# Optimization experiments

Measured on AMD Instinct MI355X. Metric: run time of the kernel, lower is better.

## Reference

```python
import jax, jax.numpy as jnp
import numpy as np

N_NODES = 100000
N_EDGES = 1600000
D_IN = 128
D_H = 128
NEG_SLOPE = 0.2  # DGL GATConv default


def gat_layer(x, W, attn_l, attn_r, bias, src, dst, n_nodes):
    # x: [N, Din] -> h: [N, H]  (num_heads=1, head dim squeezed)
    h = x @ W
    el = jnp.einsum('nh,h->n', h, attn_l)  # [N]
    er = jnp.einsum('nh,h->n', h, attn_r)  # [N]
    e = jax.nn.leaky_relu(el[src] + er[dst], NEG_SLOPE)  # [E]
    # edge softmax over incoming edges of each dst node (numerically stable)
    m = jax.ops.segment_max(e, dst, num_segments=n_nodes)  # [N], -inf on zero-in-degree
    ex = jnp.exp(e - m[dst])  # [E]
    s = jax.ops.segment_sum(ex, dst, num_segments=n_nodes)  # [N]
    a = ex / s[dst]  # [E]
    out = jax.ops.segment_sum(a[:, None] * h[src], dst, num_segments=n_nodes)  # [N, H]
    return out + bias


def setup_inputs() -> dict:
    key = jax.random.key(0)
    ks = jax.random.split(key, 16)
    feat = jax.random.normal(ks[0], (N_NODES, D_IN), dtype=jnp.float32)
    src = jax.random.randint(ks[1], (N_EDGES,), 0, N_NODES, dtype=jnp.int32)
    dst = jax.random.randint(ks[2], (N_EDGES,), 0, N_NODES, dtype=jnp.int32)
    def xavier(k, shape):
        fan = sum(shape)
        return jax.random.normal(k, shape, dtype=jnp.float32) * jnp.sqrt(2.0 / fan)
    params = {}
    dims = [D_IN, D_H, D_H]
    for i in range(3):
        params[f'W{i+1}'] = xavier(ks[3 + 4 * i], (dims[i], D_H))
        params[f'al{i+1}'] = xavier(ks[4 + 4 * i], (D_H,))
        params[f'ar{i+1}'] = xavier(ks[5 + 4 * i], (D_H,))
        params[f'b{i+1}'] = jnp.zeros((D_H,), dtype=jnp.float32)
    return dict(feat=feat, src=src, dst=dst, **params)


def reference(feat, src, dst, W1, al1, ar1, b1, W2, al2, ar2, b2, W3, al3, ar3, b3):
    n = feat.shape[0]
    h = gat_layer(feat, W1, al1, ar1, b1, src, dst, n)
    h = gat_layer(h, W2, al2, ar2, b2, src, dst, n)
    h = gat_layer(h, W3, al3, ar3, b3, src, dst, n)
    return h  # [N, H] (head dim of size 1 squeezed)
```

## Files before the change

kernel.cpp:

```cpp
#include <hip/hip_runtime.h>

#define DH 128
#define NBMAX 1024
#define BCH 16384

typedef __attribute__((ext_vector_type(8))) short s16x8;
typedef __attribute__((ext_vector_type(4))) float f32x4;
typedef __attribute__((ext_vector_type(4))) uint u32x4;

__device__ __forceinline__ ushort f2bf(float x) {
  uint u = __builtin_bit_cast(uint, x);
  u = (u + 0x7FFF + ((u >> 16) & 1)) >> 16;
  return (ushort)u;
}
__device__ __forceinline__ float bfl2f(uint u) {
  return __builtin_bit_cast(float, u << 16);
}
__device__ __forceinline__ float bfh2f(uint u) {
  return __builtin_bit_cast(float, u & 0xFFFF0000u);
}


__global__ __launch_bounds__(256) void chist_kernel(const int* __restrict__ dst,
                                                    int* __restrict__ chist, int E, int NB) {
  __shared__ int h[NBMAX];
  int t = threadIdx.x;
  for (int i = t; i < NB; i += 256) h[i] = 0;
  __syncthreads();
  int base = blockIdx.x * BCH;
  int n = min(BCH, E - base);
  for (int i = t; i < n; i += 256) atomicAdd(&h[((uint)dst[base + i]) >> 7], 1);
  __syncthreads();
  for (int i = t; i < NB; i += 256)
    if (h[i]) atomicAdd(&chist[i * 16], h[i]);
}

__global__ __launch_bounds__(256) void cscan_kernel(const int* __restrict__ chist,
                                                    int* __restrict__ cbase, int* __restrict__ ccur,
                                                    int* __restrict__ rowptr, int N, int NB, int E) {
  __shared__ int lds[256];
  int t = threadIdx.x;
  int v[4], s = 0;
#pragma unroll
  for (int j = 0; j < 4; ++j) {
    int idx = t * 4 + j;
    v[j] = (idx < NB) ? chist[idx * 16] : 0;
    s += v[j];
  }
  lds[t] = s;
  __syncthreads();
  for (int off = 1; off < 256; off <<= 1) {
    int add = (t >= off) ? lds[t - off] : 0;
    __syncthreads();
    lds[t] += add;
    __syncthreads();
  }
  int run = t ? lds[t - 1] : 0;
#pragma unroll
  for (int j = 0; j < 4; ++j) {
    int idx = t * 4 + j;
    if (idx < NB) {
      cbase[idx] = run;
      ccur[idx * 16] = run;
    }
    run += v[j];
  }
  if (t == 255) cbase[NB] = lds[255];
  if (t == 0) rowptr[N] = E;
}

__global__ __launch_bounds__(256) void binscat_kernel(const int* __restrict__ src,
                                                      const int* __restrict__ dst,
                                                      int* __restrict__ ccur,
                                                      uint* __restrict__ puv, int E, int NB) {
  __shared__ int h[NBMAX];
  __shared__ int gb[NBMAX];
  int t = threadIdx.x;
  int base = blockIdx.x * BCH;
  int n = min(BCH, E - base);
  for (int i = t; i < NB; i += 256) h[i] = 0;
  __syncthreads();
  for (int i = t; i < n; i += 256) atomicAdd(&h[((uint)dst[base + i]) >> 7], 1);
  __syncthreads();
  for (int i = t; i < NB; i += 256) {
    int c = h[i];
    gb[i] = c ? atomicAdd(&ccur[i * 16], c) : 0;
    h[i] = 0;
  }
  __syncthreads();
  for (int i = t; i < n; i += 256) {
    uint d = (uint)dst[base + i];
    int b = d >> 7;
    int p = gb[b] + atomicAdd(&h[b], 1);
    puv[p] = ((d & 127u) << 25) | (uint)src[base + i];
  }
}

__global__ __launch_bounds__(256) void finesort_kernel(const uint* __restrict__ puv,
                                                       const int* __restrict__ cbase,
                                                       int* __restrict__ rowptr,
                                                       int* __restrict__ ssrc, int N) {
  int b = blockIdx.x;
  int base = cbase[b];
  int cnt = cbase[b + 1] - base;
  __shared__ int ncnt[128], nincl[128], noff[128];
  int t = threadIdx.x;
  if (t < 128) ncnt[t] = 0;
  __syncthreads();
  for (int i = t; i < cnt; i += 256) atomicAdd(&ncnt[puv[base + i] >> 25], 1);
  __syncthreads();
  if (t < 128) nincl[t] = ncnt[t];
  __syncthreads();
  for (int off = 1; off < 128; off <<= 1) {
    int add = (t < 128 && t >= off) ? nincl[t - off] : 0;
    __syncthreads();
    if (t < 128) nincl[t] += add;
    __syncthreads();
  }
  if (t < 128) {
    noff[t] = nincl[t] - ncnt[t];
    int node = (b << 7) + t;
    if (node < N) rowptr[node] = base + noff[t];
    ncnt[t] = 0;
  }
  __syncthreads();
  for (int i = t; i < cnt; i += 256) {
    uint e = puv[base + i];
    int ln = e >> 25;
    int p = base + noff[ln] + atomicAdd(&ncnt[ln], 1);
    ssrc[p] = (int)(e & 0x1FFFFFFu);
  }
}

__global__ __launch_bounds__(256) void wt_kernel(const float* __restrict__ W0,
                                                 const float* __restrict__ W1,
                                                 const float* __restrict__ W2,
                                                 ushort* __restrict__ Wtb) {
  int b = blockIdx.x;
  int layer = b >> 6;
  const float* W = layer == 0 ? W0 : (layer == 1 ? W1 : W2);
  int i = (b & 63) * 256 + threadIdx.x;
  int col = i >> 7, k = i & 127;
  Wtb[(size_t)layer * DH * DH + (size_t)col * DH + k] = f2bf(W[(size_t)k * DH + col]);
}

template <bool XF32>
__global__ __launch_bounds__(512) void gemm_kernel(const void* __restrict__ xin,
                                                   const ushort* __restrict__ Wtb,
                                                   const float* __restrict__ al,
                                                   const float* __restrict__ ar,
                                                   ushort* __restrict__ hb,
                                                   float* __restrict__ el,
                                                   float* __restrict__ er, int M) {
  __shared__ ushort As[128 * DH];
  __shared__ ushort Bs[DH * DH];
  int t = threadIdx.x;
  int R0 = blockIdx.x * 128;

  for (int i = t; i < 2048; i += 512) {
    int col = i >> 4, kb = i & 15;
    s16x8 v = *(const s16x8*)(Wtb + (size_t)col * DH + kb * 8);
    *(s16x8*)(&Bs[col * DH + ((kb ^ (col & 15)) * 8)]) = v;
  }
  for (int i = t; i < 2048; i += 512) {
    int row = i >> 4, kb = i & 15;
    int gr = R0 + row;
    s16x8 v;
    if (gr < M) {
      if constexpr (XF32) {
        const float4* p = (const float4*)((const float*)xin + (size_t)gr * DH + kb * 8);
        float4 a = p[0], b = p[1];
        v[0] = (short)f2bf(a.x); v[1] = (short)f2bf(a.y);
        v[2] = (short)f2bf(a.z); v[3] = (short)f2bf(a.w);
        v[4] = (short)f2bf(b.x); v[5] = (short)f2bf(b.y);
        v[6] = (short)f2bf(b.z); v[7] = (short)f2bf(b.w);
      } else {
        v = *(const s16x8*)((const ushort*)xin + (size_t)gr * DH + kb * 8);
      }
    } else {
      v = (s16x8)0;
    }
    *(s16x8*)(&As[row * DH + ((kb ^ (row & 15)) * 8)]) = v;
  }
  __syncthreads();

  int w = t >> 6, lane = t & 63;
  int li = lane & 15, lq = lane >> 4;
  f32x4 acc[8] = {};
  int arow = w * 16 + li;
#pragma unroll
  for (int kc = 0; kc < 4; ++kc) {
    int kb = kc * 4 + lq;
    s16x8 af = *(const s16x8*)(&As[arow * DH + ((kb ^ (arow & 15)) * 8)]);
#pragma unroll
    for (int cf = 0; cf < 8; ++cf) {
      int bcol = cf * 16 + li;
      s16x8 bf = *(const s16x8*)(&Bs[bcol * DH + ((kb ^ (bcol & 15)) * 8)]);
      acc[cf] = __builtin_amdgcn_mfma_f32_16x16x32_bf16(af, bf, acc[cf], 0, 0, 0);
    }
  }

  int Rw = R0 + w * 16;
  float alv[8], arv[8];
#pragma unroll
  for (int cf = 0; cf < 8; ++cf) {
    alv[cf] = al[cf * 16 + li];
    arv[cf] = ar[cf * 16 + li];
  }
#pragma unroll
  for (int r = 0; r < 4; ++r) {
    float sl = 0.f, sr = 0.f;
#pragma unroll
    for (int cf = 0; cf < 8; ++cf) {
      sl += acc[cf][r] * alv[cf];
      sr += acc[cf][r] * arv[cf];
    }
#pragma unroll
    for (int off = 1; off <= 8; off <<= 1) {
      sl += __shfl_xor(sl, off);
      sr += __shfl_xor(sr, off);
    }
    int grow = Rw + lq * 4 + r;
    if (li == 0 && grow < M) {
      el[grow] = sl;
      er[grow] = sr;
    }
  }

  ushort* hl = &As[w * 16 * DH];
#pragma unroll
  for (int cf = 0; cf < 8; ++cf)
#pragma unroll
    for (int r = 0; r < 4; ++r) hl[(lq * 4 + r) * DH + cf * 16 + li] = f2bf(acc[cf][r]);
#pragma unroll
  for (int p = 0; p < 4; ++p) {
    int row = lane >> 2;
    int blk = (lane & 3) + p * 4;
    s16x8 v = *(const s16x8*)(&hl[row * DH + blk * 8]);
    int grow = Rw + row;
    if (grow < M)
      __builtin_nontemporal_store(v, (s16x8*)(hb + (size_t)grow * DH + blk * 8));
  }
}

template <int FINAL>
__global__ __launch_bounds__(256) void agg_kernel(const ushort* __restrict__ hb,
                                                  const float* __restrict__ el,
                                                  const float* __restrict__ er,
                                                  const int* __restrict__ rowptr,
                                                  const int* __restrict__ ssrc,
                                                  const float* __restrict__ bias,
                                                  void* __restrict__ outv, int M) {
  int wid = (blockIdx.x * blockDim.x + threadIdx.x) >> 6;
  int lane = threadIdx.x & 63;
  if (wid >= M) return;
  int begin = rowptr[wid], end = rowptr[wid + 1];
  int deg = end - begin;

  if (deg > 64) {
    float er_d = er[wid];
    float mx = -1e30f;
    for (int e = begin + lane; e < end; e += 64) {
      float s = el[ssrc[e]] + er_d;
      s = s > 0.f ? s : 0.2f * s;
      mx = fmaxf(mx, s);
    }
#pragma unroll
    for (int off = 32; off; off >>= 1) mx = fmaxf(mx, __shfl_xor(mx, off));
    float acc0 = 0.f, acc1 = 0.f, ssum_l = 0.f;
    for (int base = begin; base < end; base += 64) {
      int n = min(64, end - base);
      int e = base + lane;
      int idx = 0;
      float wgt = 0.f;
      if (lane < n) {
        idx = ssrc[e];
        float sc = el[idx] + er_d;
        sc = sc > 0.f ? sc : 0.2f * sc;
        wgt = __expf(sc - mx);
      }
      ssum_l += wgt;
      for (int j = 0; j < n; ++j) {
        int s = __shfl(idx, j);
        float wg = __shfl(wgt, j);
        uint u = ((const uint*)(hb + (size_t)s * DH))[lane];
        acc0 += wg * bfl2f(u);
        acc1 += wg * bfh2f(u);
      }
    }
#pragma unroll
    for (int off = 32; off; off >>= 1) ssum_l += __shfl_xor(ssum_l, off);
    float inv = 1.f / ssum_l;
    float2 b2 = ((const float2*)bias)[lane];
    float o0 = acc0 * inv + b2.x;
    float o1 = acc1 * inv + b2.y;
    if constexpr (FINAL) {
      ((float2*)((float*)outv + (size_t)wid * DH))[lane] = make_float2(o0, o1);
    } else {
      uint p = (uint)f2bf(o0) | ((uint)f2bf(o1) << 16);
      ((uint*)((ushort*)outv + (size_t)wid * DH))[lane] = p;
    }
    return;
  }

  float acc[8] = {};
  float inv = 0.f;
  if (deg > 0) {
    int e = begin + lane;
    int idx = (e < end) ? ssrc[e] : 0;
    float sc = -1e30f;
    if (e < end) {
      sc = el[idx] + er[wid];
      sc = sc > 0.f ? sc : 0.2f * sc;
    }
    float mx = sc;
#pragma unroll
    for (int off = 32; off; off >>= 1) mx = fmaxf(mx, __shfl_xor(mx, off));
    float wgt = (e < end) ? __expf(sc - mx) : 0.f;
    float ssum = wgt;
#pragma unroll
    for (int off = 32; off; off >>= 1) ssum += __shfl_xor(ssum, off);
    inv = 1.f / ssum;

    int q = lane >> 4, cl = lane & 15;
    const uint4* hb4 = (const uint4*)hb;
    for (int j = 0; j < deg; j += 16) {
      uint4 u[4];
      float wq[4];
#pragma unroll
      for (int k = 0; k < 4; ++k) {
        int ej = j + k * 4 + q;
        int s = __shfl(idx, ej);
        wq[k] = __shfl(wgt, ej);
        u[k] = hb4[(size_t)s * 16 + cl];
      }
#pragma unroll
      for (int k = 0; k < 4; ++k) {
        acc[0] += wq[k] * bfl2f(u[k].x); acc[1] += wq[k] * bfh2f(u[k].x);
        acc[2] += wq[k] * bfl2f(u[k].y); acc[3] += wq[k] * bfh2f(u[k].y);
        acc[4] += wq[k] * bfl2f(u[k].z); acc[5] += wq[k] * bfh2f(u[k].z);
        acc[6] += wq[k] * bfl2f(u[k].w); acc[7] += wq[k] * bfh2f(u[k].w);
      }
    }
#pragma unroll
    for (int i = 0; i < 8; ++i) {
      acc[i] += __shfl_xor(acc[i], 16);
      acc[i] += __shfl_xor(acc[i], 32);
    }
  }
  if (lane < 16) {
    float4 b0 = ((const float4*)bias)[lane * 2];
    float4 b1 = ((const float4*)bias)[lane * 2 + 1];
    float o[8];
    o[0] = acc[0] * inv + b0.x; o[1] = acc[1] * inv + b0.y;
    o[2] = acc[2] * inv + b0.z; o[3] = acc[3] * inv + b0.w;
    o[4] = acc[4] * inv + b1.x; o[5] = acc[5] * inv + b1.y;
    o[6] = acc[6] * inv + b1.z; o[7] = acc[7] * inv + b1.w;
    if constexpr (FINAL) {
      f32x4 p0 = {o[0], o[1], o[2], o[3]};
      f32x4 p1 = {o[4], o[5], o[6], o[7]};
      float* op = (float*)outv + (size_t)wid * DH + lane * 8;
      *(f32x4*)op = p0;
      *(f32x4*)(op + 4) = p1;
    } else {
      u32x4 p;
      p.x = (uint)f2bf(o[0]) | ((uint)f2bf(o[1]) << 16);
      p.y = (uint)f2bf(o[2]) | ((uint)f2bf(o[3]) << 16);
      p.z = (uint)f2bf(o[4]) | ((uint)f2bf(o[5]) << 16);
      p.w = (uint)f2bf(o[6]) | ((uint)f2bf(o[7]) << 16);
      __builtin_nontemporal_store(p, (u32x4*)((ushort*)outv + (size_t)wid * DH) + lane);
    }
  }
}

extern "C" void kernel_launch(void* const* d_in, const int* in_sizes, int n_in,
                              void* d_out, int out_size, void* d_ws, size_t ws_size,
                              hipStream_t stream) {
  const float* feat = (const float*)d_in[0];
  const int* src = (const int*)d_in[1];
  const int* dst = (const int*)d_in[2];
  const int N = in_sizes[0] / DH;
  const int E = in_sizes[1];
  const int NB = (N + 127) >> 7;
  const float* W[3]  = {(const float*)d_in[3], (const float*)d_in[7],  (const float*)d_in[11]};
  const float* al[3] = {(const float*)d_in[4], (const float*)d_in[8],  (const float*)d_in[12]};
  const float* ar[3] = {(const float*)d_in[5], (const float*)d_in[9],  (const float*)d_in[13]};
  const float* bi[3] = {(const float*)d_in[6], (const float*)d_in[10], (const float*)d_in[14]};

  char* ws = (char*)d_ws;
  size_t off = 0;
  auto alloc = [&](size_t bytes) {
    void* p = ws + off;
    off = (off + bytes + 255) & ~(size_t)255;
    return p;
  };
  ushort* hb   = (ushort*)alloc((size_t)N * DH * sizeof(ushort));
  ushort* xb   = (ushort*)alloc((size_t)N * DH * sizeof(ushort));
  float* el    = (float*)alloc((size_t)N * sizeof(float));
  float* er    = (float*)alloc((size_t)N * sizeof(float));
  int* rowptr  = (int*)alloc((size_t)(N + 1) * sizeof(int));
  int* ssrc    = (int*)alloc((size_t)E * sizeof(int));
  ushort* Wtb  = (ushort*)alloc((size_t)3 * DH * DH * sizeof(ushort));
  int* chist   = (int*)alloc((size_t)NBMAX * 16 * sizeof(int));
  int* cbase   = (int*)alloc((size_t)(NBMAX + 1) * sizeof(int));
  int* ccur    = (int*)alloc((size_t)NBMAX * 16 * sizeof(int));
  uint* puv    = (uint*)hb;

  hipMemsetAsync(chist, 0, (size_t)NBMAX * 16 * sizeof(int), stream);
  int ebl = (E + BCH - 1) / BCH;
  chist_kernel<<<ebl, 256, 0, stream>>>(dst, chist, E, NB);
  cscan_kernel<<<1, 256, 0, stream>>>(chist, cbase, ccur, rowptr, N, NB, E);
  binscat_kernel<<<ebl, 256, 0, stream>>>(src, dst, ccur, puv, E, NB);
  finesort_kernel<<<NB, 256, 0, stream>>>(puv, cbase, rowptr, ssrc, N);
  wt_kernel<<<192, 256, 0, stream>>>(W[0], W[1], W[2], Wtb);

  for (int l = 0; l < 3; ++l) {
    const ushort* Wl = Wtb + (size_t)l * DH * DH;
    if (l == 0)
      gemm_kernel<true><<<(N + 127) / 128, 512, 0, stream>>>(feat, Wl, al[l], ar[l], hb, el, er, N);
    else
      gemm_kernel<false><<<(N + 127) / 128, 512, 0, stream>>>(xb, Wl, al[l], ar[l], hb, el, er, N);
    if (l < 2)
      agg_kernel<0><<<(N + 3) / 4, 256, 0, stream>>>(hb, el, er, rowptr, ssrc, bi[l], xb, N);
    else
      agg_kernel<1><<<(N + 3) / 4, 256, 0, stream>>>(hb, el, er, rowptr, ssrc, bi[l], d_out, N);
  }
}
```

Before: 345.4 us.

## Fuse CSR histogram into layer-0 GEMM launch and merge prep kernels

Merges the weight transpose with the zeroing of the histogram into one prep kernel, replacing the memset. The destination histogram becomes extra blocks of the first-layer GEMM launch so the two overlap. The scatter scratch buffer moves from hb to xb so the GEMM output can be written before sorting. BCH shrinks to 4096 for more blocks, and the sort loops are unrolled to batch loads ahead of the LDS atomics. This adds kernel complexity and more global atomics on chist.

```diff
diff --git a/kernel.cpp b/kernel.cpp
--- a/kernel.cpp
+++ b/kernel.cpp
@@ -2,11 +2,12 @@
 
 #define DH 128
 #define NBMAX 1024
-#define BCH 16384
+#define BCH 4096
 
 typedef __attribute__((ext_vector_type(8))) short s16x8;
 typedef __attribute__((ext_vector_type(4))) float f32x4;
 typedef __attribute__((ext_vector_type(4))) uint u32x4;
+typedef __attribute__((ext_vector_type(4))) int i32x4;
 
 __device__ __forceinline__ ushort f2bf(float x) {
   uint u = __builtin_bit_cast(uint, x);
@@ -20,143 +21,32 @@
   return __builtin_bit_cast(float, u & 0xFFFF0000u);
 }
 
-
-__global__ __launch_bounds__(256) void chist_kernel(const int* __restrict__ dst,
-                                                    int* __restrict__ chist, int E, int NB) {
-  __shared__ int h[NBMAX];
-  int t = threadIdx.x;
-  for (int i = t; i < NB; i += 256) h[i] = 0;
-  __syncthreads();
-  int base = blockIdx.x * BCH;
-  int n = min(BCH, E - base);
-  for (int i = t; i < n; i += 256) atomicAdd(&h[((uint)dst[base + i]) >> 7], 1);
-  __syncthreads();
-  for (int i = t; i < NB; i += 256)
-    if (h[i]) atomicAdd(&chist[i * 16], h[i]);
-}
-
-__global__ __launch_bounds__(256) void cscan_kernel(const int* __restrict__ chist,
-                                                    int* __restrict__ cbase, int* __restrict__ ccur,
-                                                    int* __restrict__ rowptr, int N, int NB, int E) {
-  __shared__ int lds[256];
-  int t = threadIdx.x;
-  int v[4], s = 0;
-#pragma unroll
-  for (int j = 0; j < 4; ++j) {
-    int idx = t * 4 + j;
-    v[j] = (idx < NB) ? chist[idx * 16] : 0;
-    s += v[j];
-  }
-  lds[t] = s;
-  __syncthreads();
-  for (int off = 1; off < 256; off <<= 1) {
-    int add = (t >= off) ? lds[t - off] : 0;
-    __syncthreads();
-    lds[t] += add;
-    __syncthreads();
-  }
-  int run = t ? lds[t - 1] : 0;
-#pragma unroll
-  for (int j = 0; j < 4; ++j) {
-    int idx = t * 4 + j;
-    if (idx < NB) {
-      cbase[idx] = run;
-      ccur[idx * 16] = run;
-    }
-    run += v[j];
-  }
-  if (t == 255) cbase[NB] = lds[255];
-  if (t == 0) rowptr[N] = E;
-}
-
-__global__ __launch_bounds__(256) void binscat_kernel(const int* __restrict__ src,
-                                                      const int* __restrict__ dst,
-                                                      int* __restrict__ ccur,
-                                                      uint* __restrict__ puv, int E, int NB) {
-  __shared__ int h[NBMAX];
-  __shared__ int gb[NBMAX];
-  int t = threadIdx.x;
-  int base = blockIdx.x * BCH;
-  int n = min(BCH, E - base);
-  for (int i = t; i < NB; i += 256) h[i] = 0;
-  __syncthreads();
-  for (int i = t; i < n; i += 256) atomicAdd(&h[((uint)dst[base + i]) >> 7], 1);
-  __syncthreads();
-  for (int i = t; i < NB; i += 256) {
-    int c = h[i];
-    gb[i] = c ? atomicAdd(&ccur[i * 16], c) : 0;
-    h[i] = 0;
-  }
-  __syncthreads();
-  for (int i = t; i < n; i += 256) {
-    uint d = (uint)dst[base + i];
-    int b = d >> 7;
-    int p = gb[b] + atomicAdd(&h[b], 1);
-    puv[p] = ((d & 127u) << 25) | (uint)src[base + i];
-  }
-}
-
-__global__ __launch_bounds__(256) void finesort_kernel(const uint* __restrict__ puv,
-                                                       const int* __restrict__ cbase,
-                                                       int* __restrict__ rowptr,
-                                                       int* __restrict__ ssrc, int N) {
-  int b = blockIdx.x;
-  int base = cbase[b];
-  int cnt = cbase[b + 1] - base;
-  __shared__ int ncnt[128], nincl[128], noff[128];
-  int t = threadIdx.x;
-  if (t < 128) ncnt[t] = 0;
-  __syncthreads();
-  for (int i = t; i < cnt; i += 256) atomicAdd(&ncnt[puv[base + i] >> 25], 1);
-  __syncthreads();
-  if (t < 128) nincl[t] = ncnt[t];
-  __syncthreads();
-  for (int off = 1; off < 128; off <<= 1) {
-    int add = (t < 128 && t >= off) ? nincl[t - off] : 0;
-    __syncthreads();
-    if (t < 128) nincl[t] += add;
-    __syncthreads();
-  }
-  if (t < 128) {
-    noff[t] = nincl[t] - ncnt[t];
-    int node = (b << 7) + t;
-    if (node < N) rowptr[node] = base + noff[t];
-    ncnt[t] = 0;
-  }
-  __syncthreads();
-  for (int i = t; i < cnt; i += 256) {
-    uint e = puv[base + i];
-    int ln = e >> 25;
-    int p = base + noff[ln] + atomicAdd(&ncnt[ln], 1);
-    ssrc[p] = (int)(e & 0x1FFFFFFu);
-  }
-}
-
-__global__ __launch_bounds__(256) void wt_kernel(const float* __restrict__ W0,
-                                                 const float* __restrict__ W1,
-                                                 const float* __restrict__ W2,
-                                                 ushort* __restrict__ Wtb) {
-  int b = blockIdx.x;
-  int layer = b >> 6;
-  const float* W = layer == 0 ? W0 : (layer == 1 ? W1 : W2);
-  int i = (b & 63) * 256 + threadIdx.x;
-  int col = i >> 7, k = i & 127;
-  Wtb[(size_t)layer * DH * DH + (size_t)col * DH + k] = f2bf(W[(size_t)k * DH + col]);
+__global__ __launch_bounds__(512) void prep_kernel(const float* __restrict__ W0,
+                                                   const float* __restrict__ W1,
+                                                   const float* __restrict__ W2,
+                                                   ushort* __restrict__ Wtb,
+                                                   int* __restrict__ chist) {
+  int b = blockIdx.x, t = threadIdx.x;
+  if (b < 96) {
+    int g = b * 512 + t;
+    int layer = g >> 14, i = g & 16383;
+    const float* W = layer == 0 ? W0 : (layer == 1 ? W1 : W2);
+    int col = i >> 7, k = i & 127;
+    Wtb[(size_t)layer * DH * DH + (size_t)col * DH + k] = f2bf(W[(size_t)k * DH + col]);
+  } else {
+    int idx = ((b - 96) * 512 + t) * 4;
+    *(i32x4*)(chist + idx) = (i32x4){0, 0, 0, 0};
+  }
 }
 
 template <bool XF32>
-__global__ __launch_bounds__(512) void gemm_kernel(const void* __restrict__ xin,
-                                                   const ushort* __restrict__ Wtb,
-                                                   const float* __restrict__ al,
-                                                   const float* __restrict__ ar,
-                                                   ushort* __restrict__ hb,
-                                                   float* __restrict__ el,
-                                                   float* __restrict__ er, int M) {
-  __shared__ ushort As[128 * DH];
-  __shared__ ushort Bs[DH * DH];
-  int t = threadIdx.x;
-  int R0 = blockIdx.x * 128;
-
+__device__ __forceinline__ void gemm_body(ushort* __restrict__ As, ushort* __restrict__ Bs,
+                                          const void* __restrict__ xin,
+                                          const ushort* __restrict__ Wtb,
+                                          const float* __restrict__ al,
+                                          const float* __restrict__ ar,
+                                          ushort* __restrict__ hb, float* __restrict__ el,
+                                          float* __restrict__ er, int M, int R0, int t) {
   for (int i = t; i < 2048; i += 512) {
     int col = i >> 4, kb = i & 15;
     s16x8 v = *(const s16x8*)(Wtb + (size_t)col * DH + kb * 8);
@@ -240,6 +130,203 @@
     int grow = Rw + row;
     if (grow < M)
       __builtin_nontemporal_store(v, (s16x8*)(hb + (size_t)grow * DH + blk * 8));
+  }
+}
+
+__global__ __launch_bounds__(512) void gemm_kernel(const ushort* __restrict__ xin,
+                                                   const ushort* __restrict__ Wtb,
+                                                   const float* __restrict__ al,
+                                                   const float* __restrict__ ar,
+                                                   ushort* __restrict__ hb,
+                                                   float* __restrict__ el,
+                                                   float* __restrict__ er, int M) {
+  __shared__ ushort As[128 * DH];
+  __shared__ ushort Bs[DH * DH];
+  gemm_body<false>(As, Bs, xin, Wtb, al, ar, hb, el, er, M, blockIdx.x * 128, threadIdx.x);
+}
+
+__global__ __launch_bounds__(512) void gemm0_chist_kernel(const float* __restrict__ feat,
+                                                          const ushort* __restrict__ Wtb,
+                                                          const float* __restrict__ al,
+                                                          const float* __restrict__ ar,
+                                                          ushort* __restrict__ hb,
+                                                          float* __restrict__ el,
+                                                          float* __restrict__ er, int M,
+                                                          const int* __restrict__ dst,
+                                                          int* __restrict__ chist, int E, int NB,
+                                                          int GB) {
+  __shared__ ushort As[128 * DH];
+  __shared__ ushort Bs[DH * DH];
+  int b = blockIdx.x, t = threadIdx.x;
+  if (b < GB) {
+    gemm_body<true>(As, Bs, feat, Wtb, al, ar, hb, el, er, M, b * 128, t);
+    return;
+  }
+  int* h = (int*)As;
+  for (int i = t; i < NB; i += 512) h[i] = 0;
+  __syncthreads();
+  int base = (b - GB) * BCH;
+  int n = min(BCH, E - base);
+  for (int i0 = 0; i0 < n; i0 += 2048) {
+    uint d[4]; bool ok[4];
+#pragma unroll
+    for (int k = 0; k < 4; ++k) {
+      int i = i0 + k * 512 + t;
+      ok[k] = i < n;
+      d[k] = ok[k] ? (uint)dst[base + i] : 0u;
+    }
+#pragma unroll
+    for (int k = 0; k < 4; ++k)
+      if (ok[k]) atomicAdd(&h[d[k] >> 7], 1);
+  }
+  __syncthreads();
+  for (int i = t; i < NB; i += 512)
+    if (h[i]) atomicAdd(&chist[i * 16], h[i]);
+}
+
+__global__ __launch_bounds__(256) void cscan_kernel(const int* __restrict__ chist,
+                                                    int* __restrict__ cbase, int* __restrict__ ccur,
+                                                    int* __restrict__ rowptr, int N, int NB, int E) {
+  __shared__ int lds[256];
+  int t = threadIdx.x;
+  int v[4], s = 0;
+#pragma unroll
+  for (int j = 0; j < 4; ++j) {
+    int idx = t * 4 + j;
+    v[j] = (idx < NB) ? chist[idx * 16] : 0;
+    s += v[j];
+  }
+  lds[t] = s;
+  __syncthreads();
+  for (int off = 1; off < 256; off <<= 1) {
+    int add = (t >= off) ? lds[t - off] : 0;
+    __syncthreads();
+    lds[t] += add;
+    __syncthreads();
+  }
+  int run = t ? lds[t - 1] : 0;
+#pragma unroll
+  for (int j = 0; j < 4; ++j) {
+    int idx = t * 4 + j;
+    if (idx < NB) {
+      cbase[idx] = run;
+      ccur[idx * 16] = run;
+    }
+    run += v[j];
+  }
+  if (t == 255) cbase[NB] = lds[255];
+  if (t == 0) rowptr[N] = E;
+}
+
+__global__ __launch_bounds__(256) void binscat_kernel(const int* __restrict__ src,
+                                                      const int* __restrict__ dst,
+                                                      int* __restrict__ ccur,
+                                                      uint* __restrict__ puv, int E, int NB) {
+  __shared__ int h[NBMAX];
+  __shared__ int gb[NBMAX];
+  int t = threadIdx.x;
+  int base = blockIdx.x * BCH;
+  int n = min(BCH, E - base);
+  for (int i = t; i < NB; i += 256) h[i] = 0;
+  __syncthreads();
+  for (int i0 = 0; i0 < n; i0 += 2048) {
+    uint d[8]; bool ok[8];
+#pragma unroll
+    for (int k = 0; k < 8; ++k) {
+      int i = i0 + k * 256 + t;
+      ok[k] = i < n;
+      d[k] = ok[k] ? (uint)dst[base + i] : 0u;
+    }
+#pragma unroll
+    for (int k = 0; k < 8; ++k)
+      if (ok[k]) atomicAdd(&h[d[k] >> 7], 1);
+  }
+  __syncthreads();
+  for (int i = t; i < NB; i += 256) {
+    int c = h[i];
+    gb[i] = c ? atomicAdd(&ccur[i * 16], c) : 0;
+    h[i] = 0;
+  }
+  __syncthreads();
+  for (int i0 = 0; i0 < n; i0 += 2048) {
+    uint d[8], s[8]; bool ok[8];
+#pragma unroll
+    for (int k = 0; k < 8; ++k) {
+      int i = i0 + k * 256 + t;
+      ok[k] = i < n;
+      d[k] = ok[k] ? (uint)dst[base + i] : 0u;
+      s[k] = ok[k] ? (uint)src[base + i] : 0u;
+    }
+    int p[8];
+#pragma unroll
+    for (int k = 0; k < 8; ++k)
+      if (ok[k]) {
+        int bb = d[k] >> 7;
+        p[k] = gb[bb] + atomicAdd(&h[bb], 1);
+      }
+#pragma unroll
+    for (int k = 0; k < 8; ++k)
+      if (ok[k]) puv[p[k]] = ((d[k] & 127u) << 25) | s[k];
+  }
+}
+
+__global__ __launch_bounds__(256) void finesort_kernel(const uint* __restrict__ puv,
+                                                       const int* __restrict__ cbase,
+                                                       int* __restrict__ rowptr,
+                                                       int* __restrict__ ssrc, int N) {
+  int b = blockIdx.x;
+  int base = cbase[b];
+  int cnt = cbase[b + 1] - base;
+  __shared__ int ncnt[128], nincl[128], noff[128];
+  int t = threadIdx.x;
+  if (t < 128) ncnt[t] = 0;
+  __syncthreads();
+  for (int i0 = 0; i0 < cnt; i0 += 2048) {
+    uint e[8]; bool ok[8];
+#pragma unroll
+    for (int k = 0; k < 8; ++k) {
+      int i = i0 + k * 256 + t;
+      ok[k] = i < cnt;
+      e[k] = ok[k] ? puv[base + i] : 0u;
+    }
+#pragma unroll
+    for (int k = 0; k < 8; ++k)
+      if (ok[k]) atomicAdd(&ncnt[e[k] >> 25], 1);
+  }
+  __syncthreads();
+  if (t < 128) nincl[t] = ncnt[t];
+  __syncthreads();
+  for (int off = 1; off < 128; off <<= 1) {
+    int add = (t < 128 && t >= off) ? nincl[t - off] : 0;
+    __syncthreads();
+    if (t < 128) nincl[t] += add;
+    __syncthreads();
+  }
+  if (t < 128) {
+    noff[t] = nincl[t] - ncnt[t];
+    int node = (b << 7) + t;
+    if (node < N) rowptr[node] = base + noff[t];
+    ncnt[t] = 0;
+  }
+  __syncthreads();
+  for (int i0 = 0; i0 < cnt; i0 += 2048) {
+    uint e[8]; bool ok[8];
+#pragma unroll
+    for (int k = 0; k < 8; ++k) {
+      int i = i0 + k * 256 + t;
+      ok[k] = i < cnt;
+      e[k] = ok[k] ? puv[base + i] : 0u;
+    }
+    int p[8];
+#pragma unroll
+    for (int k = 0; k < 8; ++k)
+      if (ok[k]) {
+        int ln = e[k] >> 25;
+        p[k] = base + noff[ln] + atomicAdd(&ncnt[ln], 1);
+      }
+#pragma unroll
+    for (int k = 0; k < 8; ++k)
+      if (ok[k]) ssrc[p[k]] = (int)(e[k] & 0x1FFFFFFu);
   }
 }
 
@@ -404,25 +491,21 @@
   int* chist   = (int*)alloc((size_t)NBMAX * 16 * sizeof(int));
   int* cbase   = (int*)alloc((size_t)(NBMAX + 1) * sizeof(int));
   int* ccur    = (int*)alloc((size_t)NBMAX * 16 * sizeof(int));
-  uint* puv    = (uint*)hb;
-
-  hipMemsetAsync(chist, 0, (size_t)NBMAX * 16 * sizeof(int), stream);
+  uint* puv    = (uint*)xb;
+
   int ebl = (E + BCH - 1) / BCH;
-  chist_kernel<<<ebl, 256, 0, stream>>>(dst, chist, E, NB);
+  int GB = (N + 127) / 128;
+
+  prep_kernel<<<104, 512, 0, stream>>>(W[0], W[1], W[2], Wtb, chist);
+  gemm0_chist_kernel<<<GB + ebl, 512, 0, stream>>>(feat, Wtb, al[0], ar[0], hb, el, er, N,
+                                                   dst, chist, E, NB, GB);
   cscan_kernel<<<1, 256, 0, stream>>>(chist, cbase, ccur, rowptr, N, NB, E);
   binscat_kernel<<<ebl, 256, 0, stream>>>(src, dst, ccur, puv, E, NB);
   finesort_kernel<<<NB, 256, 0, stream>>>(puv, cbase, rowptr, ssrc, N);
-  wt_kernel<<<192, 256, 0, stream>>>(W[0], W[1], W[2], Wtb);
-
-  for (int l = 0; l < 3; ++l) {
-    const ushort* Wl = Wtb + (size_t)l * DH * DH;
-    if (l == 0)
-      gemm_kernel<true><<<(N + 127) / 128, 512, 0, stream>>>(feat, Wl, al[l], ar[l], hb, el, er, N);
-    else
-      gemm_kernel<false><<<(N + 127) / 128, 512, 0, stream>>>(xb, Wl, al[l], ar[l], hb, el, er, N);
-    if (l < 2)
-      agg_kernel<0><<<(N + 3) / 4, 256, 0, stream>>>(hb, el, er, rowptr, ssrc, bi[l], xb, N);
-    else
-      agg_kernel<1><<<(N + 3) / 4, 256, 0, stream>>>(hb, el, er, rowptr, ssrc, bi[l], d_out, N);
-  }
-}
+
+  agg_kernel<0><<<(N + 3) / 4, 256, 0, stream>>>(hb, el, er, rowptr, ssrc, bi[0], xb, N);
+  gemm_kernel<<<GB, 512, 0, stream>>>(xb, Wtb + DH * DH, al[1], ar[1], hb, el, er, N);
+  agg_kernel<0><<<(N + 3) / 4, 256, 0, stream>>>(hb, el, er, rowptr, ssrc, bi[1], xb, N);
+  gemm_kernel<<<GB, 512, 0, stream>>>(xb, Wtb + 2 * DH * DH, al[2], ar[2], hb, el, er, N);
+  agg_kernel<1><<<(N + 3) / 4, 256, 0, stream>>>(hb, el, er, rowptr, ssrc, bi[2], d_out, N);
+}
```

Result: faster. 324.7 us, median of 2 (-6.0%).
